# Kernel optimization log

Measured on AMD Instinct MI355X. Metric: run time of the kernel, lower is better.

Reference implementation:

```python
import jax, jax.numpy as jnp
import numpy as np

N = 65536          # nodes
E = 1048576        # edges (avg degree 16)
K = 5              # B-spline kernel size per dim (dim=3 -> 125 kernels)
F_IN, F_OUT = 1, 32
GRID = 32          # first sparse_voxel_max_pool: size = 1/32 -> 32^3 voxels
NUM_VOX = GRID ** 3

# enumerate the 2^3 corners of the degree-1 B-spline support
_BITS = np.array([[(b >> d) & 1 for d in range(3)] for b in range(8)], dtype=np.int32)  # [8,3]
_STRIDES = np.array([1, K, K * K], dtype=np.int32)  # kernel index strides per dim


def setup_inputs() -> dict:
    key = jax.random.key(0)
    ks = jax.random.split(key, 7)
    x = jax.random.normal(ks[0], (N, F_IN), dtype=jnp.float32)
    edge_index = jax.random.randint(ks[1], (2, E), 0, N, dtype=jnp.int32)
    pseudo = jax.random.uniform(ks[2], (E, 3), dtype=jnp.float32)   # edge pseudo-coords in [0,1]^3
    pos = jax.random.uniform(ks[3], (N, 3), dtype=jnp.float32)      # node positions in [0,1]^3
    W = jax.random.normal(ks[4], (K ** 3, F_IN, F_OUT), dtype=jnp.float32) * 0.1
    W_root = jax.random.normal(ks[5], (F_IN, F_OUT), dtype=jnp.float32) * 0.1
    bias = jax.random.normal(ks[6], (F_OUT,), dtype=jnp.float32) * 0.1
    return {"x": x, "edge_index": edge_index, "pseudo": pseudo, "pos": pos,
            "W": W, "W_root": W_root, "bias": bias}


def spline_basis(pseudo):
    """Degree-1 open B-spline basis. Returns (weights [E,8], kernel_idx [E,8])."""
    v = pseudo * (K - 1)                                   # [E,3] in [0, K-1]
    i0 = jnp.clip(jnp.floor(v), 0, K - 2)                  # lower knot per dim
    f = v - i0                                             # fractional part
    i0 = i0.astype(jnp.int32)
    bits = jnp.asarray(_BITS)                              # [8,3]
    idx = i0[:, None, :] + bits[None]                      # [E,8,3]
    w = jnp.where(bits[None].astype(bool), f[:, None, :], 1.0 - f[:, None, :])
    B = w.prod(axis=-1)                                    # [E,8]
    kidx = (idx * jnp.asarray(_STRIDES)).sum(axis=-1)      # [E,8] in [0,125)
    return B, kidx


def spline_conv(x, edge_index, pseudo, W, W_root, bias):
    src, dst = edge_index[0], edge_index[1]
    B, kidx = spline_basis(pseudo)                         # [E,8], [E,8]
    xj = x[src]                                            # [E,F_IN] edge-wise gather
    Wg = W[kidx]                                           # [E,8,F_IN,F_OUT]
    msg = jnp.einsum('es,ef,esfo->eo', B, xj, Wg)          # basis-weighted messages [E,F_OUT]
    agg = jax.ops.segment_sum(msg, dst, num_segments=N)    # scatter-add
    deg = jax.ops.segment_sum(jnp.ones((E,), jnp.float32), dst, num_segments=N)
    out = agg / jnp.clip(deg, 1.0)[:, None] + x @ W_root + bias  # mean aggr + root + bias
    return out


def reference(x, edge_index, pseudo, pos, W, W_root, bias):
    h = jax.nn.elu(spline_conv(x, edge_index, pseudo, W, W_root, bias))  # [N,32]
    # sparse voxel max pooling: hash positions to a 32^3 grid, scatter-max features
    vid = jnp.clip(jnp.floor(pos * GRID), 0, GRID - 1).astype(jnp.int32)  # [N,3]
    vidx = vid[:, 0] + GRID * vid[:, 1] + GRID * GRID * vid[:, 2]         # [N]
    pooled = jax.ops.segment_max(h, vidx, num_segments=NUM_VOX)           # [32768,32]
    pooled = jnp.where(jnp.isfinite(pooled), pooled, 0.0)                 # empty voxels -> 0
    return pooled
```

## Files before the change

kernel.cpp:

```cpp
#include <hip/hip_runtime.h>
#include <math.h>

#define F_OUT     32
#define GRID_DIM  32
#define NUM_VOX   (GRID_DIM * GRID_DIM * GRID_DIM)

#define NPB   64
#define NBKT  1024
#define SEB   1024
#define CAP   1344
#define SCS   132
#define DEGS  125
#define CSTR  32

__device__ __forceinline__ unsigned int enc_f32(float f) {
    unsigned int u = __float_as_uint(f);
    return (u & 0x80000000u) ? ~u : (u | 0x80000000u);
}
__device__ __forceinline__ float dec_f32(unsigned int e) {
    return (e & 0x80000000u) ? __uint_as_float(e ^ 0x80000000u)
                             : __uint_as_float(~e);
}

__global__ __launch_bounds__(512) void scatter_kernel(
    const int*   __restrict__ src,
    const int*   __restrict__ dst,
    const float* __restrict__ x,
    const float* __restrict__ pseudo,
    float4* __restrict__ payload,
    unsigned int* __restrict__ cursor,
    int E)
{
    __shared__ unsigned int sHist[NBKT];
    __shared__ unsigned int sCur[NBKT];

    const int t  = threadIdx.x;
    const int e0 = blockIdx.x * SEB;

    for (int i = t; i < NBKT; i += 512) sHist[i] = 0;
    __syncthreads();

    unsigned short dloc[SEB / 512];
    float4 pay[SEB / 512];
    #pragma unroll
    for (int i = 0; i < SEB / 512; ++i) {
        int e = e0 + i * 512 + t;
        if (e < E) {
            int d = dst[e];
            int s = src[e];
            float p0 = pseudo[3 * e], p1 = pseudo[3 * e + 1], p2 = pseudo[3 * e + 2];
            float xj = x[s];
            unsigned int q2 = (unsigned int)(p2 * 65535.0f + 0.5f) & 0xFFFFu;
            unsigned int w  = q2 | ((unsigned int)(d & 63) << 16);
            dloc[i] = (unsigned short)d;
            pay[i]  = make_float4(p0, p1, xj, __uint_as_float(w));
            atomicAdd(&sHist[d >> 6], 1u);
        }
    }
    __syncthreads();

    for (int b = t; b < NBKT; b += 512) {
        unsigned int c = sHist[b];
        sCur[b] = c ? atomicAdd(&cursor[(size_t)b * CSTR], c) : 0u;
    }
    __syncthreads();

    #pragma unroll
    for (int i = 0; i < SEB / 512; ++i) {
        int e = e0 + i * 512 + t;
        if (e < E) {
            unsigned int bkt  = (unsigned int)dloc[i] >> 6;
            unsigned int slot = atomicAdd(&sCur[bkt], 1u);
            if (slot < CAP)
                payload[(size_t)bkt * CAP + slot] = pay[i];
        }
    }
}

__device__ __forceinline__ void process_edge(float4 r, float* sC, int half)
{
    unsigned int w = __float_as_uint(r.w);
    int rel6 = (int)((w >> 16) & 63u);
    if ((rel6 >> 5) != half) return;

    float xj = r.z;
    float p2 = (float)(w & 0xFFFFu) * (1.0f / 65535.0f);

    float v0 = r.x * 4.0f, v1 = r.y * 4.0f, v2 = p2 * 4.0f;
    float i0 = fminf(fmaxf(floorf(v0), 0.0f), 3.0f);
    float i1 = fminf(fmaxf(floorf(v1), 0.0f), 3.0f);
    float i2 = fminf(fmaxf(floorf(v2), 0.0f), 3.0f);
    float f0 = v0 - i0, f1 = v1 - i1, f2 = v2 - i2;
    float g0 = 1.0f - f0, g1 = 1.0f - f1, g2 = 1.0f - f2;
    int k = (int)i0 + 5 * (int)i1 + 25 * (int)i2;

    float w00 = g0 * g1, w10 = f0 * g1, w01 = g0 * f1, w11 = f0 * f1;
    float a2 = xj * g2, b2 = xj * f2;
    float* row = sC + (rel6 & 31) * SCS;
    atomicAdd(row + k +  0, w00 * a2);
    atomicAdd(row + k +  1, w10 * a2);
    atomicAdd(row + k +  5, w01 * a2);
    atomicAdd(row + k +  6, w11 * a2);
    atomicAdd(row + k + 25, w00 * b2);
    atomicAdd(row + k + 26, w10 * b2);
    atomicAdd(row + k + 30, w01 * b2);
    atomicAdd(row + k + 31, w11 * b2);
    atomicAdd(row + DEGS, 1.0f);
}

__global__ __launch_bounds__(256) void owner_kernel(
    const float4* __restrict__ payload,
    const unsigned int* __restrict__ cursor,
    const float* __restrict__ W,
    const float* __restrict__ x,
    const float* __restrict__ W_root,
    const float* __restrict__ bias,
    const float* __restrict__ pos,
    unsigned int* __restrict__ pooled,
    int Nn)
{
    __shared__ __align__(16) float sC[32 * SCS];

    const int t    = threadIdx.x;
    const int bp   = blockIdx.x;
    const int b    = bp >> 1;
    const int half = bp & 1;

    for (int i = t; i < 32 * SCS / 4; i += 256)
        *(float4*)&sC[i * 4] = make_float4(0.f, 0.f, 0.f, 0.f);
    __syncthreads();

    int cnt = (int)cursor[(size_t)b * CSTR];
    if (cnt > CAP) cnt = CAP;
    const float4* slab = payload + (size_t)b * CAP;
    {
        int i = t;
        if (i < cnt) {
            float4 r = slab[i];
            for (i += 256; i < cnt; i += 256) {
                float4 rn = slab[i];
                process_edge(r, sC, half);
                r = rn;
            }
            process_edge(r, sC, half);
        }
    }
    __syncthreads();

    const int node = t & 31;
    const int cg   = t >> 5;
    const float* crow = sC + node * SCS;
    float4 acc = make_float4(0.f, 0.f, 0.f, 0.f);
    #pragma unroll 8
    for (int k4 = 0; k4 < 31; ++k4) {
        float4 r = *(const float4*)&crow[k4 * 4];
        const float* wp = W + (k4 * 4) * F_OUT + cg * 4;
        float4 w0 = *(const float4*)(wp);
        float4 w1 = *(const float4*)(wp + F_OUT);
        float4 w2 = *(const float4*)(wp + 2 * F_OUT);
        float4 w3 = *(const float4*)(wp + 3 * F_OUT);
        acc.x += r.x * w0.x + r.y * w1.x + r.z * w2.x + r.w * w3.x;
        acc.y += r.x * w0.y + r.y * w1.y + r.z * w2.y + r.w * w3.y;
        acc.z += r.x * w0.z + r.y * w1.z + r.z * w2.z + r.w * w3.z;
        acc.w += r.x * w0.w + r.y * w1.w + r.z * w2.w + r.w * w3.w;
    }
    {
        float r = crow[124];
        const float* wp = W + 124 * F_OUT + cg * 4;
        acc.x += r * wp[0]; acc.y += r * wp[1];
        acc.z += r * wp[2]; acc.w += r * wp[3];
    }
    float dg = fmaxf(crow[DEGS], 1.0f);
    int   n  = b * NPB + half * 32 + node;
    float xn = (n < Nn) ? x[n] : 0.0f;
    float4 wr = *(const float4*)(W_root + cg * 4);
    float4 bs = *(const float4*)(bias + cg * 4);
    __syncthreads();

    if (n < Nn) {
        float h;
        h = acc.x / dg + xn * wr.x + bs.x; h = h > 0.f ? h : expm1f(h); sC[node * SCS + cg * 4 + 0] = h;
        h = acc.y / dg + xn * wr.y + bs.y; h = h > 0.f ? h : expm1f(h); sC[node * SCS + cg * 4 + 1] = h;
        h = acc.z / dg + xn * wr.z + bs.z; h = h > 0.f ? h : expm1f(h); sC[node * SCS + cg * 4 + 2] = h;
        h = acc.w / dg + xn * wr.w + bs.w; h = h > 0.f ? h : expm1f(h); sC[node * SCS + cg * 4 + 3] = h;
    }
    __syncthreads();

    for (int item = t; item < 32 * F_OUT; item += 256) {
        int nr = item >> 5, o = item & 31;
        int nn = b * NPB + half * 32 + nr;
        if (nn >= Nn) break;
        int vx = min(max((int)floorf(pos[3 * nn + 0] * (float)GRID_DIM), 0), GRID_DIM - 1);
        int vy = min(max((int)floorf(pos[3 * nn + 1] * (float)GRID_DIM), 0), GRID_DIM - 1);
        int vz = min(max((int)floorf(pos[3 * nn + 2] * (float)GRID_DIM), 0), GRID_DIM - 1);
        int vidx = vx + GRID_DIM * vy + GRID_DIM * GRID_DIM * vz;
        atomicMax(&pooled[(size_t)vidx * F_OUT + o], enc_f32(sC[nr * SCS + o]));
    }
}

__global__ __launch_bounds__(256) void finalize_kernel(
    const unsigned int* pooled,
    float* out, int M)
{
    int i = blockIdx.x * blockDim.x + threadIdx.x;
    if (i >= M) return;
    unsigned int u = pooled[i];
    out[i] = (u == 0u) ? 0.0f : dec_f32(u);
}

extern "C" void kernel_launch(void* const* d_in, const int* in_sizes, int n_in,
                              void* d_out, int out_size, void* d_ws, size_t ws_size,
                              hipStream_t stream) {
    const float* x       = (const float*)d_in[0];
    const int*   ei      = (const int*)  d_in[1];
    const float* pseudo  = (const float*)d_in[2];
    const float* pos     = (const float*)d_in[3];
    const float* W       = (const float*)d_in[4];
    const float* W_root  = (const float*)d_in[5];
    const float* bias    = (const float*)d_in[6];

    const int E   = in_sizes[1] / 2;
    const int Nn  = in_sizes[0];
    const int nSB = (E + SEB - 1) / SEB;
    const int nb  = 2 * ((Nn + NPB - 1) / NPB);

    float4*       payload = (float4*)d_ws;
    unsigned int* cursor  = (unsigned int*)((char*)d_ws + (size_t)NBKT * CAP * sizeof(float4));

    unsigned int* pooled = (unsigned int*)d_out;
    const int M = (out_size < NUM_VOX * F_OUT) ? out_size : NUM_VOX * F_OUT;

    hipMemsetAsync(cursor, 0, (size_t)NBKT * CSTR * sizeof(unsigned int), stream);
    hipMemsetAsync(d_out, 0, (size_t)M * sizeof(float), stream);

    scatter_kernel<<<nSB, 512, 0, stream>>>(ei, ei + E, x, pseudo, payload, cursor, E);
    owner_kernel<<<nb, 256, 0, stream>>>(payload, cursor, W, x, W_root, bias, pos,
                                         pooled, Nn);
    finalize_kernel<<<(M + 255) / 256, 256, 0, stream>>>(pooled, (float*)d_out, M);
}
```

Measured before the change: 186.0 us.

## Coarsen dst buckets to 256 nodes and stage scatter payload in LDS for coalesced writes

The scatter kernel now buckets edges into 256 groups of 256 destination nodes instead of 1024 groups of 64. It sorts each block's 2048 edges by group in shared memory using a wave prefix scan, then writes the payload to global memory contiguously, so stores are coalesced instead of being scattered per edge. The owner kernel handles 128 nodes per half-block, with a 128-row shared accumulator and four output tiles per thread. This cuts global cursor atomics and scatter write cost, but raises shared memory use per block (about 67KB in the owner kernel), which lowers occupancy, and each owner block now reads and filters a bucket twice as large.

After: 179.4 us. -3.5%, faster.

```diff
diff --git a/kernel.cpp b/kernel.cpp
--- a/kernel.cpp
+++ b/kernel.cpp
@@ -5,10 +5,12 @@
 #define GRID_DIM  32
 #define NUM_VOX   (GRID_DIM * GRID_DIM * GRID_DIM)
 
-#define NPB   64
-#define NBKT  1024
-#define SEB   1024
-#define CAP   1344
+#define NGRP  256
+#define GNPB  256
+#define HNPB  128
+#define SEB   2048
+#define EPT   4
+#define BCAP  4480
 #define SCS   132
 #define DEGS  125
 #define CSTR  32
@@ -31,57 +33,90 @@
     unsigned int* __restrict__ cursor,
     int E)
 {
-    __shared__ unsigned int sHist[NBKT];
-    __shared__ unsigned int sCur[NBKT];
+    __shared__ unsigned int sHist[NGRP];
+    __shared__ unsigned int sStart[NGRP];
+    __shared__ unsigned int sGBase[NGRP];
+    __shared__ unsigned int sTotal;
+    __shared__ unsigned short sGid[SEB];
+    __shared__ __align__(16) float4 sPay[SEB];
 
     const int t  = threadIdx.x;
     const int e0 = blockIdx.x * SEB;
 
-    for (int i = t; i < NBKT; i += 512) sHist[i] = 0;
-    __syncthreads();
-
-    unsigned short dloc[SEB / 512];
-    float4 pay[SEB / 512];
+    if (t < NGRP) sHist[t] = 0;
+    __syncthreads();
+
+    unsigned short dloc[EPT];
+    float4 pay[EPT];
+    bool   val[EPT];
     #pragma unroll
-    for (int i = 0; i < SEB / 512; ++i) {
+    for (int i = 0; i < EPT; ++i) {
         int e = e0 + i * 512 + t;
-        if (e < E) {
+        val[i] = (e < E);
+        if (val[i]) {
             int d = dst[e];
             int s = src[e];
             float p0 = pseudo[3 * e], p1 = pseudo[3 * e + 1], p2 = pseudo[3 * e + 2];
             float xj = x[s];
             unsigned int q2 = (unsigned int)(p2 * 65535.0f + 0.5f) & 0xFFFFu;
-            unsigned int w  = q2 | ((unsigned int)(d & 63) << 16);
+            pay[i]  = make_float4(p0, p1, xj,
+                        __uint_as_float(q2 | ((unsigned int)(d & 255) << 16)));
             dloc[i] = (unsigned short)d;
-            pay[i]  = make_float4(p0, p1, xj, __uint_as_float(w));
-            atomicAdd(&sHist[d >> 6], 1u);
-        }
-    }
-    __syncthreads();
-
-    for (int b = t; b < NBKT; b += 512) {
-        unsigned int c = sHist[b];
-        sCur[b] = c ? atomicAdd(&cursor[(size_t)b * CSTR], c) : 0u;
+            atomicAdd(&sHist[(d >> 8) & 255], 1u);
+        } else dloc[i] = 0;
+    }
+    __syncthreads();
+
+    if (t < 64) {
+        unsigned int c0 = sHist[4*t], c1 = sHist[4*t+1], c2 = sHist[4*t+2], c3 = sHist[4*t+3];
+        unsigned int loc = c0 + c1 + c2 + c3;
+        unsigned int incl = loc;
+        #pragma unroll
+        for (int d = 1; d < 64; d <<= 1) {
+            unsigned int v = __shfl_up(incl, d, 64);
+            if (t >= d) incl += v;
+        }
+        unsigned int excl = incl - loc;
+        sStart[4*t]   = excl;
+        sStart[4*t+1] = excl + c0;
+        sStart[4*t+2] = excl + c0 + c1;
+        sStart[4*t+3] = excl + c0 + c1 + c2;
+        if (t == 63) sTotal = incl;
+    }
+    __syncthreads();
+
+    if (t < NGRP) {
+        unsigned int c = sHist[t];
+        sGBase[t] = c ? atomicAdd(&cursor[(size_t)t * CSTR], c) : 0u;
+        sHist[t]  = sStart[t];
     }
     __syncthreads();
 
     #pragma unroll
-    for (int i = 0; i < SEB / 512; ++i) {
-        int e = e0 + i * 512 + t;
-        if (e < E) {
-            unsigned int bkt  = (unsigned int)dloc[i] >> 6;
-            unsigned int slot = atomicAdd(&sCur[bkt], 1u);
-            if (slot < CAP)
-                payload[(size_t)bkt * CAP + slot] = pay[i];
-        }
+    for (int i = 0; i < EPT; ++i) {
+        if (val[i]) {
+            unsigned int g = ((unsigned int)dloc[i] >> 8) & 255u;
+            unsigned int slot = atomicAdd(&sHist[g], 1u);
+            sPay[slot] = pay[i];
+            sGid[slot] = (unsigned short)g;
+        }
+    }
+    __syncthreads();
+
+    const unsigned int total = sTotal;
+    for (unsigned int i = t; i < total; i += 512) {
+        unsigned int g   = sGid[i];
+        unsigned int idx = sGBase[g] + (i - sStart[g]);
+        if (idx < BCAP)
+            payload[(size_t)g * BCAP + idx] = sPay[i];
     }
 }
 
 __device__ __forceinline__ void process_edge(float4 r, float* sC, int half)
 {
     unsigned int w = __float_as_uint(r.w);
-    int rel6 = (int)((w >> 16) & 63u);
-    if ((rel6 >> 5) != half) return;
+    int rel8 = (int)((w >> 16) & 255u);
+    if ((rel8 >> 7) != half) return;
 
     float xj = r.z;
     float p2 = (float)(w & 0xFFFFu) * (1.0f / 65535.0f);
@@ -96,7 +131,7 @@
 
     float w00 = g0 * g1, w10 = f0 * g1, w01 = g0 * f1, w11 = f0 * f1;
     float a2 = xj * g2, b2 = xj * f2;
-    float* row = sC + (rel6 & 31) * SCS;
+    float* row = sC + (rel8 & 127) * SCS;
     atomicAdd(row + k +  0, w00 * a2);
     atomicAdd(row + k +  1, w10 * a2);
     atomicAdd(row + k +  5, w01 * a2);
@@ -119,20 +154,20 @@
     unsigned int* __restrict__ pooled,
     int Nn)
 {
-    __shared__ __align__(16) float sC[32 * SCS];
+    __shared__ __align__(16) float sC[HNPB * SCS];
 
     const int t    = threadIdx.x;
-    const int bp   = blockIdx.x;
-    const int b    = bp >> 1;
-    const int half = bp & 1;
-
-    for (int i = t; i < 32 * SCS / 4; i += 256)
-        *(float4*)&sC[i * 4] = make_float4(0.f, 0.f, 0.f, 0.f);
-    __syncthreads();
-
-    int cnt = (int)cursor[(size_t)b * CSTR];
-    if (cnt > CAP) cnt = CAP;
-    const float4* slab = payload + (size_t)b * CAP;
+    const int g    = blockIdx.x >> 1;
+    const int half = blockIdx.x & 1;
+
+    for (int i = t; i < HNPB * SCS / 4; i += 256)
+        ((float4*)sC)[i] = make_float4(0.f, 0.f, 0.f, 0.f);
+
+    int cnt = (int)cursor[(size_t)g * CSTR];
+    if (cnt > BCAP) cnt = BCAP;
+    const float4* slab = payload + (size_t)g * BCAP;
+    __syncthreads();
+
     {
         int i = t;
         if (i < cnt) {
@@ -147,49 +182,53 @@
     }
     __syncthreads();
 
-    const int node = t & 31;
-    const int cg   = t >> 5;
-    const float* crow = sC + node * SCS;
-    float4 acc = make_float4(0.f, 0.f, 0.f, 0.f);
-    #pragma unroll 8
-    for (int k4 = 0; k4 < 31; ++k4) {
-        float4 r = *(const float4*)&crow[k4 * 4];
-        const float* wp = W + (k4 * 4) * F_OUT + cg * 4;
-        float4 w0 = *(const float4*)(wp);
-        float4 w1 = *(const float4*)(wp + F_OUT);
-        float4 w2 = *(const float4*)(wp + 2 * F_OUT);
-        float4 w3 = *(const float4*)(wp + 3 * F_OUT);
-        acc.x += r.x * w0.x + r.y * w1.x + r.z * w2.x + r.w * w3.x;
-        acc.y += r.x * w0.y + r.y * w1.y + r.z * w2.y + r.w * w3.y;
-        acc.z += r.x * w0.z + r.y * w1.z + r.z * w2.z + r.w * w3.z;
-        acc.w += r.x * w0.w + r.y * w1.w + r.z * w2.w + r.w * w3.w;
-    }
-    {
-        float r = crow[124];
-        const float* wp = W + 124 * F_OUT + cg * 4;
-        acc.x += r * wp[0]; acc.y += r * wp[1];
-        acc.z += r * wp[2]; acc.w += r * wp[3];
-    }
-    float dg = fmaxf(crow[DEGS], 1.0f);
-    int   n  = b * NPB + half * 32 + node;
-    float xn = (n < Nn) ? x[n] : 0.0f;
-    float4 wr = *(const float4*)(W_root + cg * 4);
-    float4 bs = *(const float4*)(bias + cg * 4);
-    __syncthreads();
-
-    if (n < Nn) {
-        float h;
-        h = acc.x / dg + xn * wr.x + bs.x; h = h > 0.f ? h : expm1f(h); sC[node * SCS + cg * 4 + 0] = h;
-        h = acc.y / dg + xn * wr.y + bs.y; h = h > 0.f ? h : expm1f(h); sC[node * SCS + cg * 4 + 1] = h;
-        h = acc.z / dg + xn * wr.z + bs.z; h = h > 0.f ? h : expm1f(h); sC[node * SCS + cg * 4 + 2] = h;
-        h = acc.w / dg + xn * wr.w + bs.w; h = h > 0.f ? h : expm1f(h); sC[node * SCS + cg * 4 + 3] = h;
-    }
-    __syncthreads();
-
-    for (int item = t; item < 32 * F_OUT; item += 256) {
+    const int nl = t & 31;
+    const int cg = t >> 5;
+    const float4 wr = *(const float4*)(W_root + cg * 4);
+    const float4 bs = *(const float4*)(bias + cg * 4);
+
+    #pragma unroll
+    for (int tile = 0; tile < 4; ++tile) {
+        const int node = tile * 32 + nl;
+        const float* crow = sC + node * SCS;
+        float4 acc = make_float4(0.f, 0.f, 0.f, 0.f);
+        #pragma unroll 8
+        for (int k4 = 0; k4 < 31; ++k4) {
+            float4 r = *(const float4*)&crow[k4 * 4];
+            const float* wp = W + (k4 * 4) * F_OUT + cg * 4;
+            float4 w0 = *(const float4*)(wp);
+            float4 w1 = *(const float4*)(wp + F_OUT);
+            float4 w2 = *(const float4*)(wp + 2 * F_OUT);
+            float4 w3 = *(const float4*)(wp + 3 * F_OUT);
+            acc.x += r.x * w0.x + r.y * w1.x + r.z * w2.x + r.w * w3.x;
+            acc.y += r.x * w0.y + r.y * w1.y + r.z * w2.y + r.w * w3.y;
+            acc.z += r.x * w0.z + r.y * w1.z + r.z * w2.z + r.w * w3.z;
+            acc.w += r.x * w0.w + r.y * w1.w + r.z * w2.w + r.w * w3.w;
+        }
+        {
+            float r = crow[124];
+            const float* wp = W + 124 * F_OUT + cg * 4;
+            acc.x += r * wp[0]; acc.y += r * wp[1];
+            acc.z += r * wp[2]; acc.w += r * wp[3];
+        }
+        float dg = fmaxf(crow[DEGS], 1.0f);
+        int   n  = g * GNPB + half * HNPB + node;
+        float xn = (n < Nn) ? x[n] : 0.0f;
+        __syncthreads();
+        if (n < Nn) {
+            float h;
+            h = acc.x / dg + xn * wr.x + bs.x; h = h > 0.f ? h : expm1f(h); sC[node * SCS + cg * 4 + 0] = h;
+            h = acc.y / dg + xn * wr.y + bs.y; h = h > 0.f ? h : expm1f(h); sC[node * SCS + cg * 4 + 1] = h;
+            h = acc.z / dg + xn * wr.z + bs.z; h = h > 0.f ? h : expm1f(h); sC[node * SCS + cg * 4 + 2] = h;
+            h = acc.w / dg + xn * wr.w + bs.w; h = h > 0.f ? h : expm1f(h); sC[node * SCS + cg * 4 + 3] = h;
+        }
+    }
+    __syncthreads();
+
+    for (int item = t; item < HNPB * F_OUT; item += 256) {
         int nr = item >> 5, o = item & 31;
-        int nn = b * NPB + half * 32 + nr;
-        if (nn >= Nn) break;
+        int nn = g * GNPB + half * HNPB + nr;
+        if (nn >= Nn) continue;
         int vx = min(max((int)floorf(pos[3 * nn + 0] * (float)GRID_DIM), 0), GRID_DIM - 1);
         int vy = min(max((int)floorf(pos[3 * nn + 1] * (float)GRID_DIM), 0), GRID_DIM - 1);
         int vz = min(max((int)floorf(pos[3 * nn + 2] * (float)GRID_DIM), 0), GRID_DIM - 1);
@@ -219,18 +258,18 @@
     const float* W_root  = (const float*)d_in[5];
     const float* bias    = (const float*)d_in[6];
 
-    const int E   = in_sizes[1] / 2;
-    const int Nn  = in_sizes[0];
-    const int nSB = (E + SEB - 1) / SEB;
-    const int nb  = 2 * ((Nn + NPB - 1) / NPB);
+    const int E    = in_sizes[1] / 2;
+    const int Nn   = in_sizes[0];
+    const int nSB  = (E + SEB - 1) / SEB;
+    const int nb   = 2 * ((Nn + GNPB - 1) / GNPB);
 
     float4*       payload = (float4*)d_ws;
-    unsigned int* cursor  = (unsigned int*)((char*)d_ws + (size_t)NBKT * CAP * sizeof(float4));
+    unsigned int* cursor  = (unsigned int*)((char*)d_ws + (size_t)NGRP * BCAP * sizeof(float4));
 
     unsigned int* pooled = (unsigned int*)d_out;
     const int M = (out_size < NUM_VOX * F_OUT) ? out_size : NUM_VOX * F_OUT;
 
-    hipMemsetAsync(cursor, 0, (size_t)NBKT * CSTR * sizeof(unsigned int), stream);
+    hipMemsetAsync(cursor, 0, (size_t)NGRP * CSTR * sizeof(unsigned int), stream);
     hipMemsetAsync(d_out, 0, (size_t)M * sizeof(float), stream);
 
     scatter_kernel<<<nSB, 512, 0, stream>>>(ei, ei + E, x, pseudo, payload, cursor, E);
```
